# Kernel tuning notes

Measured on AMD Instinct MI355X. Metric: run time of the kernel, lower is better.

## Reference

```python
import jax, jax.numpy as jnp
import numpy as np

# tf.image.rgb_to_grayscale luminance weights
_RGB_W = jnp.array([0.2989, 0.5870, 0.1140], dtype=jnp.float32)
# LBP weight kernel (row-major over the 3x3 neighborhood)
_LBP_K = jnp.array([[1.0, 2.0, 4.0],
                    [128.0, 0.0, 8.0],
                    [64.0, 32.0, 16.0]], dtype=jnp.float32)


def setup_inputs() -> dict:
    key = jax.random.key(0)
    inputs = jax.random.uniform(key, (32, 512, 512, 3), dtype=jnp.float32)
    return {"inputs": inputs}


def reference(inputs):
    # inputs: [N, H, W, 3]
    gray = jnp.tensordot(inputs, _RGB_W, axes=[[-1], [0]])  # [N, H, W]
    N, H, W = gray.shape
    padded = jnp.pad(gray, ((0, 0), (1, 1), (1, 1)))  # SAME zero padding
    # extract_patches(3x3, SAME) -> 9 channels in row-major (dy, dx) order
    patches = jnp.stack(
        [padded[:, dy:dy + H, dx:dx + W] for dy in range(3) for dx in range(3)],
        axis=-1,
    )  # [N, H, W, 9]
    center = patches[..., 4:5]
    binary = jnp.where(patches >= center, 1.0, 0.0)  # [N, H, W, 9]
    # Original conv2d tiles the SAME 3x3 spatial kernel across all 9 input
    # channels, so it equals: (sum over channels) then a 3x3 weighted sum.
    s = binary.sum(axis=-1)  # [N, H, W]
    sp = jnp.pad(s, ((0, 0), (1, 1), (1, 1)))  # SAME zero padding for conv
    lbp = sum(
        _LBP_K[dy, dx] * sp[:, dy:dy + H, dx:dx + W]
        for dy in range(3) for dx in range(3)
        if _LBP_K[dy, dx] != 0.0
    )
    return lbp[..., None]  # [N, H, W, 1]
```

## Files before the change

### kernel.cpp

```cpp
#include <hip/hip_runtime.h>


#define TPB    256
#define TILE_X 64
#define TILE_Y 32
#define GROWS  36
#define GCOLS  72
#define SROWS  34
#define SCOLS  68
#define GQ     (GROWS * (GCOLS / 4))
#define SQ     (SROWS * (SCOLS / 4))

typedef float f32x4 __attribute__((ext_vector_type(4)));

template<bool EDGE>
__device__ __forceinline__ void do_tile(const float* __restrict__ in,
                                        float* __restrict__ out,
                                        float* __restrict__ grayS,
                                        float* __restrict__ sS,
                                        int n, int y0, int x0, int tid) {
    #pragma unroll
    for (int k = 0; k < 3; ++k) {
        const int i = tid + k * TPB;
        if (i < GQ) {
            const int qy  = i / (GCOLS / 4);
            const int qx  = i - qy * (GCOLS / 4);
            const int gy  = y0 - 2 + qy;
            const int px0 = x0 - 4 + qx * 4;
            int cy = gy, cx = px0;
            bool ok = true;
            if (EDGE) {
                const bool oky = (unsigned)gy  < 512u;
                const bool okx = (unsigned)px0 < 512u;
                ok = oky & okx;
                cy = min(max(gy, 0), 511);
                cx = okx ? px0 : 0;
            }
            const f32x4* p4 = reinterpret_cast<const f32x4*>(
                in + ((size_t)(n * 512 + cy) * 512 + (size_t)cx) * 3);
            const f32x4 f0 = p4[0];
            const f32x4 f1 = p4[1];
            const f32x4 f2 = p4[2];
            float g0 = __builtin_fmaf(f0.z, 0.114f, __builtin_fmaf(f0.y, 0.587f, f0.x * 0.2989f));
            float g1 = __builtin_fmaf(f1.y, 0.114f, __builtin_fmaf(f1.x, 0.587f, f0.w * 0.2989f));
            float g2 = __builtin_fmaf(f2.x, 0.114f, __builtin_fmaf(f1.w, 0.587f, f1.z * 0.2989f));
            float g3 = __builtin_fmaf(f2.w, 0.114f, __builtin_fmaf(f2.z, 0.587f, f2.y * 0.2989f));
            f32x4 gv;
            if (EDGE) {
                gv.x = ok ? g0 : 0.0f;
                gv.y = ok ? g1 : 0.0f;
                gv.z = ok ? g2 : 0.0f;
                gv.w = ok ? g3 : 0.0f;
            } else {
                gv.x = g0; gv.y = g1; gv.z = g2; gv.w = g3;
            }
            *reinterpret_cast<f32x4*>(&grayS[qy * GCOLS + qx * 4]) = gv;
        }
    }
    __syncthreads();

    #pragma unroll
    for (int k = 0; k < 3; ++k) {
        const int i = tid + k * TPB;
        if (i < SQ) {
            const int ly  = i / (SCOLS / 4);
            const int lx0 = (i - ly * (SCOLS / 4)) * 4;
            const f32x4 a0 = *reinterpret_cast<const f32x4*>(&grayS[(ly + 0) * GCOLS + lx0]);
            const f32x4 b0 = *reinterpret_cast<const f32x4*>(&grayS[(ly + 0) * GCOLS + lx0 + 4]);
            const f32x4 a1 = *reinterpret_cast<const f32x4*>(&grayS[(ly + 1) * GCOLS + lx0]);
            const f32x4 b1 = *reinterpret_cast<const f32x4*>(&grayS[(ly + 1) * GCOLS + lx0 + 4]);
            const f32x4 a2 = *reinterpret_cast<const f32x4*>(&grayS[(ly + 2) * GCOLS + lx0]);
            const f32x4 b2 = *reinterpret_cast<const f32x4*>(&grayS[(ly + 2) * GCOLS + lx0 + 4]);
            const float r0[8] = {a0.x, a0.y, a0.z, a0.w, b0.x, b0.y, b0.z, b0.w};
            const float r1[8] = {a1.x, a1.y, a1.z, a1.w, b1.x, b1.y, b1.z, b1.w};
            const float r2[8] = {a2.x, a2.y, a2.z, a2.w, b2.x, b2.y, b2.z, b2.w};
            float sv[4];
            #pragma unroll
            for (int e = 0; e < 4; ++e) {
                const float c = r1[3 + e];
                unsigned su = 0;
                #pragma unroll
                for (int d = 0; d < 3; ++d) {
                    su += (r0[2 + e + d] >= c);
                    su += (r1[2 + e + d] >= c);
                    su += (r2[2 + e + d] >= c);
                }
                float s = (float)su;
                if (EDGE) {
                    const bool ok = ((unsigned)(y0 - 1 + ly) < 512u) &
                                    ((unsigned)(x0 - 1 + lx0 + e) < 512u);
                    s = ok ? s : 0.0f;
                }
                sv[e] = s;
            }
            f32x4 svv;
            svv.x = sv[0]; svv.y = sv[1]; svv.z = sv[2]; svv.w = sv[3];
            *reinterpret_cast<f32x4*>(&sS[ly * SCOLS + lx0]) = svv;
        }
    }
    __syncthreads();

    #pragma unroll
    for (int k = 0; k < 2; ++k) {
        const int i   = tid + k * TPB;
        const int py  = i / (TILE_X / 4);
        const int px0 = (i - py * (TILE_X / 4)) * 4;
        const f32x4 a0 = *reinterpret_cast<const f32x4*>(&sS[(py + 0) * SCOLS + px0]);
        const f32x4 b0 = *reinterpret_cast<const f32x4*>(&sS[(py + 0) * SCOLS + px0 + 4]);
        const f32x4 a1 = *reinterpret_cast<const f32x4*>(&sS[(py + 1) * SCOLS + px0]);
        const f32x4 b1 = *reinterpret_cast<const f32x4*>(&sS[(py + 1) * SCOLS + px0 + 4]);
        const f32x4 a2 = *reinterpret_cast<const f32x4*>(&sS[(py + 2) * SCOLS + px0]);
        const f32x4 b2 = *reinterpret_cast<const f32x4*>(&sS[(py + 2) * SCOLS + px0 + 4]);
        const float r0[8] = {a0.x, a0.y, a0.z, a0.w, b0.x, b0.y, b0.z, b0.w};
        const float r1[8] = {a1.x, a1.y, a1.z, a1.w, b1.x, b1.y, b1.z, b1.w};
        const float r2[8] = {a2.x, a2.y, a2.z, a2.w, b2.x, b2.y, b2.z, b2.w};
        f32x4 ov;
        #pragma unroll
        for (int e = 0; e < 4; ++e) {
            float acc = __builtin_fmaf(2.0f,   r0[e + 1], r0[e]);
            acc = __builtin_fmaf(4.0f,   r0[e + 2], acc);
            acc = __builtin_fmaf(128.0f, r1[e],     acc);
            acc = __builtin_fmaf(8.0f,   r1[e + 2], acc);
            acc = __builtin_fmaf(64.0f,  r2[e],     acc);
            acc = __builtin_fmaf(32.0f,  r2[e + 1], acc);
            acc = __builtin_fmaf(16.0f,  r2[e + 2], acc);
            ov[e] = acc;
        }
        f32x4* dst = reinterpret_cast<f32x4*>(
            out + (size_t)(n * 512 + (y0 + py)) * 512 + (size_t)(x0 + px0));
        __builtin_nontemporal_store(ov, dst);
    }
}

__global__ __launch_bounds__(TPB) void lbp_kernel(const float* __restrict__ in,
                                                  float* __restrict__ out) {
    __shared__ float grayS[GROWS * GCOLS];
    __shared__ float sS[SROWS * SCOLS];

    const int n  = blockIdx.z;
    const int y0 = blockIdx.y * TILE_Y;
    const int x0 = blockIdx.x * TILE_X;
    const bool edge = (blockIdx.x == 0) | (blockIdx.x == gridDim.x - 1) |
                      (blockIdx.y == 0) | (blockIdx.y == gridDim.y - 1);
    if (edge)
        do_tile<true>(in, out, grayS, sS, n, y0, x0, threadIdx.x);
    else
        do_tile<false>(in, out, grayS, sS, n, y0, x0, threadIdx.x);
}

extern "C" void kernel_launch(void* const* d_in, const int* in_sizes, int n_in,
                              void* d_out, int out_size, void* d_ws, size_t ws_size,
                              hipStream_t stream) {
    const float* in = (const float*)d_in[0];
    float* out = (float*)d_out;
    dim3 grid(512 / TILE_X, 512 / TILE_Y, 32);
    dim3 block(TPB);
    lbp_kernel<<<grid, block, 0, stream>>>(in, out);
}
```

Measured before the change: 31.06 us.

## Stage raw RGB tile into LDS via direct global_load_lds and remap blocks for XCD locality

Replaces per-thread vector global loads of RGB pixels with direct global-to-LDS async loads (global_load_lds, 16 bytes per lane) that fill a raw 36x256-float staging buffer. Grayscale conversion then reads from LDS, and the gray tile overwrites the same buffer after an extra barrier. A 1D grid with a swizzled block id is added so that consecutive blocks on each XCD handle neighbouring tiles, which is meant to improve L2 reuse of halo rows. The cost is larger LDS use (about 36 KB per block), which lowers occupancy, plus one more synchronisation.

```diff
diff --git a/kernel.cpp b/kernel.cpp
--- a/kernel.cpp
+++ b/kernel.cpp
@@ -10,51 +10,78 @@
 #define SCOLS  68
 #define GQ     (GROWS * (GCOLS / 4))
 #define SQ     (SROWS * (SCOLS / 4))
+#define RAW_FLOATS (GROWS * 256)
+#define S_OFF  (GROWS * GCOLS)
 
 typedef float f32x4 __attribute__((ext_vector_type(4)));
 
 template<bool EDGE>
 __device__ __forceinline__ void do_tile(const float* __restrict__ in,
                                         float* __restrict__ out,
-                                        float* __restrict__ grayS,
-                                        float* __restrict__ sS,
+                                        float* __restrict__ buf,
                                         int n, int y0, int x0, int tid) {
+    float* grayS = buf;
+    float* sS    = buf + S_OFF;
+
+    {
+        const int r0   = tid >> 6;
+        const int col0 = (tid & 63) * 16;
+        long gcb = (long)(x0 - 4) * 12 + col0;
+        if (EDGE) gcb = gcb < 0 ? 0 : (gcb > 6128 ? 6128 : gcb);
+        const char* base = (const char*)in;
+        #pragma unroll
+        for (int j = 0; j < 9; ++j) {
+            int gy = y0 - 2 + r0 + 4 * j;
+            if (EDGE) gy = min(max(gy, 0), 511);
+            const char* ga = base + (size_t)(n * 512 + gy) * 6144 + gcb;
+            char* la = (char*)buf + (size_t)(tid >> 6) * 1024 + (size_t)j * 4096;
+            __builtin_amdgcn_global_load_lds(
+                (const __attribute__((address_space(1))) void*)(const void*)ga,
+                (__attribute__((address_space(3))) void*)(void*)la,
+                16, 0, 0);
+        }
+    }
+    __syncthreads();
+
+    f32x4 gv[3];
     #pragma unroll
     for (int k = 0; k < 3; ++k) {
         const int i = tid + k * TPB;
         if (i < GQ) {
-            const int qy  = i / (GCOLS / 4);
-            const int qx  = i - qy * (GCOLS / 4);
-            const int gy  = y0 - 2 + qy;
-            const int px0 = x0 - 4 + qx * 4;
-            int cy = gy, cx = px0;
-            bool ok = true;
-            if (EDGE) {
-                const bool oky = (unsigned)gy  < 512u;
-                const bool okx = (unsigned)px0 < 512u;
-                ok = oky & okx;
-                cy = min(max(gy, 0), 511);
-                cx = okx ? px0 : 0;
-            }
-            const f32x4* p4 = reinterpret_cast<const f32x4*>(
-                in + ((size_t)(n * 512 + cy) * 512 + (size_t)cx) * 3);
-            const f32x4 f0 = p4[0];
-            const f32x4 f1 = p4[1];
-            const f32x4 f2 = p4[2];
+            const int qy = i / (GCOLS / 4);
+            const int qx = i - qy * (GCOLS / 4);
+            const float* rp = buf + qy * 256 + qx * 12;
+            const f32x4 f0 = *reinterpret_cast<const f32x4*>(rp);
+            const f32x4 f1 = *reinterpret_cast<const f32x4*>(rp + 4);
+            const f32x4 f2 = *reinterpret_cast<const f32x4*>(rp + 8);
             float g0 = __builtin_fmaf(f0.z, 0.114f, __builtin_fmaf(f0.y, 0.587f, f0.x * 0.2989f));
             float g1 = __builtin_fmaf(f1.y, 0.114f, __builtin_fmaf(f1.x, 0.587f, f0.w * 0.2989f));
             float g2 = __builtin_fmaf(f2.x, 0.114f, __builtin_fmaf(f1.w, 0.587f, f1.z * 0.2989f));
             float g3 = __builtin_fmaf(f2.w, 0.114f, __builtin_fmaf(f2.z, 0.587f, f2.y * 0.2989f));
-            f32x4 gv;
+            f32x4 g;
             if (EDGE) {
-                gv.x = ok ? g0 : 0.0f;
-                gv.y = ok ? g1 : 0.0f;
-                gv.z = ok ? g2 : 0.0f;
-                gv.w = ok ? g3 : 0.0f;
+                const int gy  = y0 - 2 + qy;
+                const int px0 = x0 - 4 + qx * 4;
+                const bool ok = ((unsigned)gy < 512u) & ((unsigned)px0 < 512u);
+                g.x = ok ? g0 : 0.0f;
+                g.y = ok ? g1 : 0.0f;
+                g.z = ok ? g2 : 0.0f;
+                g.w = ok ? g3 : 0.0f;
             } else {
-                gv.x = g0; gv.y = g1; gv.z = g2; gv.w = g3;
+                g.x = g0; g.y = g1; g.z = g2; g.w = g3;
             }
-            *reinterpret_cast<f32x4*>(&grayS[qy * GCOLS + qx * 4]) = gv;
+            gv[k] = g;
+        }
+    }
+    __syncthreads();
+
+    #pragma unroll
+    for (int k = 0; k < 3; ++k) {
+        const int i = tid + k * TPB;
+        if (i < GQ) {
+            const int qy = i / (GCOLS / 4);
+            const int qx = i - qy * (GCOLS / 4);
+            *reinterpret_cast<f32x4*>(&grayS[qy * GCOLS + qx * 4]) = gv[k];
         }
     }
     __syncthreads();
@@ -134,18 +161,20 @@
 
 __global__ __launch_bounds__(TPB) void lbp_kernel(const float* __restrict__ in,
                                                   float* __restrict__ out) {
-    __shared__ float grayS[GROWS * GCOLS];
-    __shared__ float sS[SROWS * SCOLS];
+    __shared__ float buf[RAW_FLOATS];
 
-    const int n  = blockIdx.z;
-    const int y0 = blockIdx.y * TILE_Y;
-    const int x0 = blockIdx.x * TILE_X;
-    const bool edge = (blockIdx.x == 0) | (blockIdx.x == gridDim.x - 1) |
-                      (blockIdx.y == 0) | (blockIdx.y == gridDim.y - 1);
+    const int id  = blockIdx.x;
+    const int nid = (id & 7) * 512 + (id >> 3);
+    const int n   = nid >> 7;
+    const int by  = (nid >> 3) & 15;
+    const int bx  = nid & 7;
+    const int y0  = by * TILE_Y;
+    const int x0  = bx * TILE_X;
+    const bool edge = (bx == 0) | (bx == 7) | (by == 0) | (by == 15);
     if (edge)
-        do_tile<true>(in, out, grayS, sS, n, y0, x0, threadIdx.x);
+        do_tile<true>(in, out, buf, n, y0, x0, threadIdx.x);
     else
-        do_tile<false>(in, out, grayS, sS, n, y0, x0, threadIdx.x);
+        do_tile<false>(in, out, buf, n, y0, x0, threadIdx.x);
 }
 
 extern "C" void kernel_launch(void* const* d_in, const int* in_sizes, int n_in,
@@ -153,7 +182,5 @@
                               hipStream_t stream) {
     const float* in = (const float*)d_in[0];
     float* out = (float*)d_out;
-    dim3 grid(512 / TILE_X, 512 / TILE_Y, 32);
-    dim3 block(TPB);
-    lbp_kernel<<<grid, block, 0, stream>>>(in, out);
+    lbp_kernel<<<dim3(4096), dim3(TPB), 0, stream>>>(in, out);
 }
```

Result: faster. 28.28 us (-8.9%).
